# Performance work log

Hardware: AMD Instinct MI355X
Metric: run time of the kernel (lower is better)

The kernel has to match this reference:

```python
import jax, jax.numpy as jnp
import numpy as np

B, T, RNN_DIM, EMB_DIM, ATT_DIM = 64, 2048, 1024, 512, 128
N_FILT, KSIZE = 32, 31
PAD = (KSIZE - 1) // 2


def setup_inputs() -> dict:
    key = jax.random.key(0)
    ks = jax.random.split(key, 9)
    return {
        "attention_hidden_state": jax.random.normal(ks[0], (B, RNN_DIM), jnp.float32),
        "memory": jax.random.normal(ks[1], (B, T, EMB_DIM), jnp.float32),
        "processed_memory": jax.random.normal(ks[2], (B, T, ATT_DIM), jnp.float32),
        "attention_weights_cat": jax.random.uniform(ks[3], (B, 2, T), jnp.float32),
        "mask": jnp.zeros((B, T), dtype=bool),
        # learned params (torch Linear stores weight as (out, in))
        "Wq": jax.random.normal(ks[4], (ATT_DIM, RNN_DIM), jnp.float32) * 0.02,
        "conv_w": jax.random.normal(ks[5], (N_FILT, 2, KSIZE), jnp.float32) * 0.1,
        "Wd": jax.random.normal(ks[6], (ATT_DIM, N_FILT), jnp.float32) * 0.1,
        "v": jax.random.normal(ks[7], (1, ATT_DIM), jnp.float32) * 0.1,
    }


def reference(attention_hidden_state, memory, processed_memory,
              attention_weights_cat, mask, Wq, conv_w, Wd, v):
    # processed_query: (B, 1, ATT_DIM)
    pq = jnp.einsum('br,ar->ba', attention_hidden_state, Wq)[:, None, :]
    # location conv: (B, 2, T) -> (B, N_FILT, T), padding keeps length
    loc = jax.lax.conv_general_dilated(
        attention_weights_cat, conv_w,
        window_strides=(1,), padding=[(PAD, PAD)],
        dimension_numbers=('NCH', 'OIH', 'NCH'))
    # transpose to (B, T, N_FILT), dense to (B, T, ATT_DIM)
    loc = jnp.einsum('bft,af->bta', loc, Wd)
    # energies: tanh(pq + loc + pm) @ v^T -> (B, T)
    energies = jnp.einsum('bta,a->bt', jnp.tanh(pq + loc + processed_memory), v[0])
    energies = jnp.where(mask, -jnp.inf, energies)
    attention_weights = jax.nn.softmax(energies, axis=1)
    # context: (B, 1, T) x (B, T, EMB) -> (B, EMB)
    attention_context = jnp.einsum('bt,bte->be', attention_weights, memory)
    return attention_context, attention_weights
```

## Files before the change

### kernel.cpp

```cpp
#include <hip/hip_runtime.h>
#include <hip/hip_bf16.h>
#include <cstdint>

#define BB 64
#define TN 2048
#define RNN 1024
#define EMB 512
#define ATT 128
#define NF 32
#define KS 31
#define PADK 15
#define CKN 62
#define ETT 256
#define CHK 32
#define NTILE (TN / ETT)

__device__ __forceinline__ float fast_rcp(float x) {
#if __has_builtin(__builtin_amdgcn_rcpf)
    return __builtin_amdgcn_rcpf(x);
#else
    return 1.0f / x;
#endif
}

__device__ __forceinline__ float fast_tanh(float x) {
    float s = __expf(2.0f * x);
    return 1.0f - 2.0f * fast_rcp(s + 1.0f);
}

__global__ __launch_bounds__(256) void prep_kernel(
    const float* __restrict__ ahs, const float* __restrict__ Wq,
    const float* __restrict__ conv_w, const float* __restrict__ Wd,
    float* __restrict__ ws_pq, float* __restrict__ ws_UT)
{
    int tid = threadIdx.x;
    if (blockIdx.x < BB) {
        int b = blockIdx.x;
        __shared__ float sh[RNN];
        for (int i = tid; i < RNN; i += 256) sh[i] = ahs[b * RNN + i];
        __syncthreads();
        int a = tid & 127, half = tid >> 7;
        const float4* wq4 = (const float4*)(Wq + a * RNN + half * (RNN / 2));
        const float4* sh4 = (const float4*)(sh + half * (RNN / 2));
        float acc = 0.0f;
#pragma unroll 8
        for (int i = 0; i < RNN / 8; ++i) {
            float4 w4 = wq4[i]; float4 h4 = sh4[i];
            acc = fmaf(w4.x, h4.x, acc);
            acc = fmaf(w4.y, h4.y, acc);
            acc = fmaf(w4.z, h4.z, acc);
            acc = fmaf(w4.w, h4.w, acc);
        }
        __shared__ float part[256];
        part[tid] = acc;
        __syncthreads();
        if (half == 0) ws_pq[b * ATT + a] = part[a] + part[a + 128];
    } else {
        __shared__ float sWd[ATT * NF];
        __shared__ float sCw[NF * CKN];
        for (int i = tid; i < ATT * NF; i += 256) sWd[i] = Wd[i];
        for (int i = tid; i < NF * CKN; i += 256) sCw[i] = conv_w[i];
        __syncthreads();
        for (int idx = tid; idx < ATT * CKN; idx += 256) {
            int a = idx & 127, ck = idx >> 7;
            float acc = 0.0f;
#pragma unroll
            for (int f = 0; f < NF; ++f) acc = fmaf(sWd[a * NF + f], sCw[f * CKN + ck], acc);
            ws_UT[idx] = acc;
        }
    }
}

__global__ __launch_bounds__(256) void fused_kernel(
    const float* __restrict__ awc, const float* __restrict__ pm,
    const float* __restrict__ vvec, const uint8_t* __restrict__ mask,
    const float* __restrict__ mem,
    const float* __restrict__ ws_pq, const float* __restrict__ ws_UT,
    float* __restrict__ ws_e, float* __restrict__ ws_mt,
    float* __restrict__ ws_st, float* __restrict__ ws_cpart)
{
    __shared__ __align__(16) float sA[2][ETT + 32];
    __shared__ float sEc[2][CHK];
    __shared__ float sEsum[CHK];
    __shared__ float4 sacc[128];

    int tid = threadIdx.x;
    int b = blockIdx.x, tile = blockIdx.y, t0 = tile * ETT;

    for (int idx = tid; idx < 2 * (ETT + 30); idx += 256) {
        int c = idx / (ETT + 30), tt = idx % (ETT + 30);
        int t = t0 + tt - PADK;
        sA[c][tt] = (t >= 0 && t < TN) ? awc[(b * 2 + c) * TN + t] : 0.0f;
    }

    int lane = tid & 63, w = tid >> 6;
    int h = w & 1, seg = w >> 1;
    int a = h * 64 + lane;

    float U[CKN];
#pragma unroll
    for (int k = 0; k < CKN; ++k) U[k] = ws_UT[k * ATT + a];
    float q = ws_pq[b * ATT + a];
    float vv = vvec[a];
    const float* pmb = pm + (size_t)b * TN * ATT + a;
    const float4* m4 = (const float4*)(mem + (size_t)(b * TN + t0) * EMB);
    int e4 = tid & 127, sub = tid >> 7;

    float m_run = -1e30f, s_run = 0.0f;
    float4 acc = make_float4(0.f, 0.f, 0.f, 0.f);
    __syncthreads();

    for (int c = 0; c < ETT / CHK; ++c) {
        int cb = c * CHK;
#pragma unroll
        for (int g = 0; g < 4; ++g) {
            int tl = cb + seg * 16 + g * 4;
            const float4* a0 = (const float4*)(&sA[0][tl]);
            const float4* a1 = (const float4*)(&sA[1][tl]);
            float x0[36], x1[36];
#pragma unroll
            for (int j = 0; j < 9; ++j) {
                float4 r0 = a0[j], r1 = a1[j];
                x0[4 * j] = r0.x; x0[4 * j + 1] = r0.y; x0[4 * j + 2] = r0.z; x0[4 * j + 3] = r0.w;
                x1[4 * j] = r1.x; x1[4 * j + 1] = r1.y; x1[4 * j + 2] = r1.z; x1[4 * j + 3] = r1.w;
            }
            float p[4];
#pragma unroll
            for (int u = 0; u < 4; ++u) p[u] = pmb[(size_t)(t0 + tl + u) * ATT];
#pragma unroll
            for (int u = 0; u < 4; ++u) {
                float lo = 0.0f;
#pragma unroll
                for (int k = 0; k < KS; ++k) {
                    lo = fmaf(U[k],      x0[u + k], lo);
                    lo = fmaf(U[KS + k], x1[u + k], lo);
                }
                float e = vv * fast_tanh(q + lo + p[u]);
#pragma unroll
                for (int off = 32; off >= 1; off >>= 1) e += __shfl_xor(e, off, 64);
                if (lane == 0) sEc[h][seg * 16 + g * 4 + u] = e;
            }
        }
        __syncthreads();
        if (tid < CHK) {
            float e = sEc[0][tid] + sEc[1][tid];
            if (mask[(size_t)b * TN + t0 + cb + tid]) e = -1e30f;
            sEsum[tid] = e;
            ws_e[(size_t)b * TN + t0 + cb + tid] = e;
        }
        __syncthreads();
        float m_new = m_run;
#pragma unroll
        for (int i = 0; i < CHK; ++i) m_new = fmaxf(m_new, sEsum[i]);
        float scl = __expf(m_run - m_new);
        float s_add = 0.0f;
#pragma unroll
        for (int i = 0; i < CHK; ++i) s_add += __expf(sEsum[i] - m_new);
        s_run = fmaf(s_run, scl, s_add);
        acc.x *= scl; acc.y *= scl; acc.z *= scl; acc.w *= scl;
        m_run = m_new;
        for (int i = sub; i < CHK; i += 2) {
            float wt = __expf(sEsum[i] - m_new);
            float4 mv = m4[(size_t)(cb + i) * 128 + e4];
            acc.x = fmaf(wt, mv.x, acc.x);
            acc.y = fmaf(wt, mv.y, acc.y);
            acc.z = fmaf(wt, mv.z, acc.z);
            acc.w = fmaf(wt, mv.w, acc.w);
        }
        __syncthreads();
    }

    if (sub == 1) sacc[e4] = acc;
    __syncthreads();
    if (sub == 0) {
        float4 o = sacc[e4];
        acc.x += o.x; acc.y += o.y; acc.z += o.z; acc.w += o.w;
        ((float4*)&ws_cpart[((size_t)tile * BB + b) * EMB])[e4] = acc;
        if (tid == 0) {
            ws_mt[tile * BB + b] = m_run;
            ws_st[tile * BB + b] = s_run;
        }
    }
}

__global__ __launch_bounds__(256) void weights_kernel(
    const float* __restrict__ ws_e, const float* __restrict__ ws_mt,
    const float* __restrict__ ws_st, float* __restrict__ out_w)
{
    int b = blockIdx.x, tid = threadIdx.x;
    float m = -1e30f;
#pragma unroll
    for (int t = 0; t < NTILE; ++t) m = fmaxf(m, ws_mt[t * BB + b]);
    float S = 0.0f;
#pragma unroll
    for (int t = 0; t < NTILE; ++t) S += ws_st[t * BB + b] * __expf(ws_mt[t * BB + b] - m);
    float inv = 1.0f / S;
#pragma unroll
    for (int i = 0; i < TN / 256; ++i) {
        int t = tid + i * 256;
        out_w[(size_t)b * TN + t] = __expf(ws_e[(size_t)b * TN + t] - m) * inv;
    }
}

__global__ __launch_bounds__(256) void ctx_reduce_kernel(
    const float* __restrict__ ws_cpart, const float* __restrict__ ws_mt,
    const float* __restrict__ ws_st, float* __restrict__ out_ctx)
{
    int o = blockIdx.x * 256 + threadIdx.x;
    int b = o >> 9, e = o & 511;
    float m = -1e30f;
#pragma unroll
    for (int t = 0; t < NTILE; ++t) m = fmaxf(m, ws_mt[t * BB + b]);
    float S = 0.0f, acc = 0.0f;
#pragma unroll
    for (int t = 0; t < NTILE; ++t) {
        float f = __expf(ws_mt[t * BB + b] - m);
        S += ws_st[t * BB + b] * f;
        acc += ws_cpart[((size_t)t * BB + b) * EMB + e] * f;
    }
    out_ctx[o] = acc / S;
}

extern "C" void kernel_launch(void* const* d_in, const int* in_sizes, int n_in,
                              void* d_out, int out_size, void* d_ws, size_t ws_size,
                              hipStream_t stream) {
    const float*   ahs  = (const float*)d_in[0];
    const float*   mem  = (const float*)d_in[1];
    const float*   pm   = (const float*)d_in[2];
    const float*   awc  = (const float*)d_in[3];
    const uint8_t* mask = (const uint8_t*)d_in[4];
    const float*   Wq   = (const float*)d_in[5];
    const float*   cw   = (const float*)d_in[6];
    const float*   Wd   = (const float*)d_in[7];
    const float*   v    = (const float*)d_in[8];

    float* out_ctx = (float*)d_out;
    float* out_w   = (float*)d_out + BB * EMB;

    float* ws       = (float*)d_ws;
    float* ws_pq    = ws;
    float* ws_UT    = ws + 8192;
    float* ws_e     = ws + 16384;
    float* ws_mt    = ws + 147456;
    float* ws_st    = ws + 147968;
    float* ws_cpart = ws + 148480;

    prep_kernel<<<BB + 1, 256, 0, stream>>>(ahs, Wq, cw, Wd, ws_pq, ws_UT);
    fused_kernel<<<dim3(BB, NTILE), 256, 0, stream>>>(
        awc, pm, v, mask, mem, ws_pq, ws_UT, ws_e, ws_mt, ws_st, ws_cpart);
    weights_kernel<<<BB, 256, 0, stream>>>(ws_e, ws_mt, ws_st, out_w);
    ctx_reduce_kernel<<<(BB * EMB) / 256, 256, 0, stream>>>(ws_cpart, ws_mt, ws_st, out_ctx);
}
```

Measured before the change: 490.8 us.

## Halve tile size and replace chunked online softmax with single-pass tile softmax

Tiles shrink from 256 to 128 timesteps, doubling the grid to 64x16 blocks. The per-chunk online-softmax loop, with its repeated barriers and serial max/sum scans over shared memory, becomes one pass: compute all energies, reduce max and sum with wave shuffles, store the weights in shared memory, then do a single memory-weighted accumulation. Each wave now handles 8 timesteps per group instead of 4, which raises register pressure (x0/x1 arrays of 40 floats each). The cost is more partial tiles for the cross-tile reduction kernels and more workspace for the partial results.

```diff
diff --git a/kernel.cpp b/kernel.cpp
--- a/kernel.cpp
+++ b/kernel.cpp
@@ -11,9 +11,9 @@
 #define KS 31
 #define PADK 15
 #define CKN 62
-#define ETT 256
-#define CHK 32
+#define ETT 128
 #define NTILE (TN / ETT)
+#define GRP 8
 
 __device__ __forceinline__ float fast_rcp(float x) {
 #if __has_builtin(__builtin_amdgcn_rcpf)
@@ -79,9 +79,10 @@
     float* __restrict__ ws_e, float* __restrict__ ws_mt,
     float* __restrict__ ws_st, float* __restrict__ ws_cpart)
 {
-    __shared__ __align__(16) float sA[2][ETT + 32];
-    __shared__ float sEc[2][CHK];
-    __shared__ float sEsum[CHK];
+    __shared__ __align__(16) float sA[2][ETT + 40];
+    __shared__ float sEc[2][ETT];
+    __shared__ float sw[ETT];
+    __shared__ float sM[2], sS[2];
     __shared__ float4 sacc[128];
 
     int tid = threadIdx.x;
@@ -103,83 +104,82 @@
     float q = ws_pq[b * ATT + a];
     float vv = vvec[a];
     const float* pmb = pm + (size_t)b * TN * ATT + a;
+    __syncthreads();
+
+    for (int g = 0; g < (ETT / 2) / GRP; ++g) {
+        int tl = seg * (ETT / 2) + g * GRP;
+        const float4* a0 = (const float4*)(&sA[0][tl]);
+        const float4* a1 = (const float4*)(&sA[1][tl]);
+        float x0[40], x1[40];
+#pragma unroll
+        for (int j = 0; j < 10; ++j) {
+            float4 r0 = a0[j], r1 = a1[j];
+            x0[4 * j] = r0.x; x0[4 * j + 1] = r0.y; x0[4 * j + 2] = r0.z; x0[4 * j + 3] = r0.w;
+            x1[4 * j] = r1.x; x1[4 * j + 1] = r1.y; x1[4 * j + 2] = r1.z; x1[4 * j + 3] = r1.w;
+        }
+        float p[GRP];
+#pragma unroll
+        for (int u = 0; u < GRP; ++u) p[u] = pmb[(size_t)(t0 + tl + u) * ATT];
+#pragma unroll
+        for (int u = 0; u < GRP; ++u) {
+            float lo = 0.0f;
+#pragma unroll
+            for (int k = 0; k < KS; ++k) {
+                lo = fmaf(U[k],      x0[u + k], lo);
+                lo = fmaf(U[KS + k], x1[u + k], lo);
+            }
+            float e = vv * fast_tanh(q + lo + p[u]);
+#pragma unroll
+            for (int off = 32; off >= 1; off >>= 1) e += __shfl_xor(e, off, 64);
+            if (lane == 0) sEc[h][tl + u] = e;
+        }
+    }
+    __syncthreads();
+
+    float e = 0.0f;
+    if (tid < ETT) {
+        e = sEc[0][tid] + sEc[1][tid];
+        if (mask[(size_t)b * TN + t0 + tid]) e = -1e30f;
+        ws_e[(size_t)b * TN + t0 + tid] = e;
+        float mloc = e;
+#pragma unroll
+        for (int off = 32; off >= 1; off >>= 1) mloc = fmaxf(mloc, __shfl_xor(mloc, off, 64));
+        if (lane == 0) sM[w] = mloc;
+    }
+    __syncthreads();
+    float m_t = fmaxf(sM[0], sM[1]);
+    if (tid < ETT) {
+        float wgt = __expf(e - m_t);
+        sw[tid] = wgt;
+        float sloc = wgt;
+#pragma unroll
+        for (int off = 32; off >= 1; off >>= 1) sloc += __shfl_xor(sloc, off, 64);
+        if (lane == 0) sS[w] = sloc;
+    }
+    __syncthreads();
+
+    int e4 = tid & 127, sub = tid >> 7;
     const float4* m4 = (const float4*)(mem + (size_t)(b * TN + t0) * EMB);
-    int e4 = tid & 127, sub = tid >> 7;
-
-    float m_run = -1e30f, s_run = 0.0f;
     float4 acc = make_float4(0.f, 0.f, 0.f, 0.f);
-    __syncthreads();
-
-    for (int c = 0; c < ETT / CHK; ++c) {
-        int cb = c * CHK;
-#pragma unroll
-        for (int g = 0; g < 4; ++g) {
-            int tl = cb + seg * 16 + g * 4;
-            const float4* a0 = (const float4*)(&sA[0][tl]);
-            const float4* a1 = (const float4*)(&sA[1][tl]);
-            float x0[36], x1[36];
-#pragma unroll
-            for (int j = 0; j < 9; ++j) {
-                float4 r0 = a0[j], r1 = a1[j];
-                x0[4 * j] = r0.x; x0[4 * j + 1] = r0.y; x0[4 * j + 2] = r0.z; x0[4 * j + 3] = r0.w;
-                x1[4 * j] = r1.x; x1[4 * j + 1] = r1.y; x1[4 * j + 2] = r1.z; x1[4 * j + 3] = r1.w;
-            }
-            float p[4];
-#pragma unroll
-            for (int u = 0; u < 4; ++u) p[u] = pmb[(size_t)(t0 + tl + u) * ATT];
-#pragma unroll
-            for (int u = 0; u < 4; ++u) {
-                float lo = 0.0f;
-#pragma unroll
-                for (int k = 0; k < KS; ++k) {
-                    lo = fmaf(U[k],      x0[u + k], lo);
-                    lo = fmaf(U[KS + k], x1[u + k], lo);
-                }
-                float e = vv * fast_tanh(q + lo + p[u]);
-#pragma unroll
-                for (int off = 32; off >= 1; off >>= 1) e += __shfl_xor(e, off, 64);
-                if (lane == 0) sEc[h][seg * 16 + g * 4 + u] = e;
-            }
-        }
-        __syncthreads();
-        if (tid < CHK) {
-            float e = sEc[0][tid] + sEc[1][tid];
-            if (mask[(size_t)b * TN + t0 + cb + tid]) e = -1e30f;
-            sEsum[tid] = e;
-            ws_e[(size_t)b * TN + t0 + cb + tid] = e;
-        }
-        __syncthreads();
-        float m_new = m_run;
-#pragma unroll
-        for (int i = 0; i < CHK; ++i) m_new = fmaxf(m_new, sEsum[i]);
-        float scl = __expf(m_run - m_new);
-        float s_add = 0.0f;
-#pragma unroll
-        for (int i = 0; i < CHK; ++i) s_add += __expf(sEsum[i] - m_new);
-        s_run = fmaf(s_run, scl, s_add);
-        acc.x *= scl; acc.y *= scl; acc.z *= scl; acc.w *= scl;
-        m_run = m_new;
-        for (int i = sub; i < CHK; i += 2) {
-            float wt = __expf(sEsum[i] - m_new);
-            float4 mv = m4[(size_t)(cb + i) * 128 + e4];
-            acc.x = fmaf(wt, mv.x, acc.x);
-            acc.y = fmaf(wt, mv.y, acc.y);
-            acc.z = fmaf(wt, mv.z, acc.z);
-            acc.w = fmaf(wt, mv.w, acc.w);
-        }
-        __syncthreads();
-    }
-
+#pragma unroll 4
+    for (int i = sub; i < ETT; i += 2) {
+        float wt = sw[i];
+        float4 mv = m4[(size_t)i * 128 + e4];
+        acc.x = fmaf(wt, mv.x, acc.x);
+        acc.y = fmaf(wt, mv.y, acc.y);
+        acc.z = fmaf(wt, mv.z, acc.z);
+        acc.w = fmaf(wt, mv.w, acc.w);
+    }
     if (sub == 1) sacc[e4] = acc;
     __syncthreads();
     if (sub == 0) {
         float4 o = sacc[e4];
         acc.x += o.x; acc.y += o.y; acc.z += o.z; acc.w += o.w;
         ((float4*)&ws_cpart[((size_t)tile * BB + b) * EMB])[e4] = acc;
-        if (tid == 0) {
-            ws_mt[tile * BB + b] = m_run;
-            ws_st[tile * BB + b] = s_run;
-        }
+    }
+    if (tid == 0) {
+        ws_mt[tile * BB + b] = m_t;
+        ws_st[tile * BB + b] = sS[0] + sS[1];
     }
 }
 
@@ -242,8 +242,8 @@
     float* ws_UT    = ws + 8192;
     float* ws_e     = ws + 16384;
     float* ws_mt    = ws + 147456;
-    float* ws_st    = ws + 147968;
-    float* ws_cpart = ws + 148480;
+    float* ws_st    = ws + 148480;
+    float* ws_cpart = ws + 149504;
 
     prep_kernel<<<BB + 1, 256, 0, stream>>>(ahs, Wq, cw, Wd, ws_pq, ws_UT);
     fused_kernel<<<dim3(BB, NTILE), 256, 0, stream>>>(
```

Result: faster. 467.4 us (-4.8%).
